# Performance work log

Measured on AMD Instinct MI355X. Metric: run time of the kernel, lower is better.

## Reference

```python
import jax, jax.numpy as jnp
import numpy as np

B, T, E, R, A, M = 64, 2000, 512, 1024, 512, 8


def setup_inputs() -> dict:
    key = jax.random.key(0)
    ks = jax.random.split(key, 9)
    attention_hidden_state = jax.random.normal(ks[0], (B, R), dtype=jnp.float32)
    memory = jax.random.normal(ks[1], (B, T, E), dtype=jnp.float32)
    previous_location = jax.random.uniform(ks[2], (B, 1, M), dtype=jnp.float32) * 10.0
    mask = jnp.zeros((B, T), dtype=bool)
    # F = Linear(R->A, bias, xavier tanh) -> Linear(A->A, no bias, xavier tanh) -> tanh -> lin(A->3M, bias)
    g = 5.0 / 3.0  # tanh gain
    lim1 = g * np.sqrt(6.0 / (R + A))
    W1 = jax.random.uniform(ks[3], (A, R), minval=-lim1, maxval=lim1, dtype=jnp.float32)
    b1 = jnp.zeros((A,), dtype=jnp.float32)
    lim2 = g * np.sqrt(6.0 / (A + A))
    W2 = jax.random.uniform(ks[4], (A, A), minval=-lim2, maxval=lim2, dtype=jnp.float32)
    lim3 = np.sqrt(1.0 / A)
    Wlin = jax.random.uniform(ks[5], (3 * M, A), minval=-lim3, maxval=lim3, dtype=jnp.float32) * 0.01
    blin = jax.random.uniform(ks[6], (3 * M,), minval=-lim3, maxval=lim3, dtype=jnp.float32) * 0.008 - 2.0
    return {"attention_hidden_state": attention_hidden_state, "memory": memory,
            "previous_location": previous_location, "mask": mask,
            "W1": W1, "b1": b1, "W2": W2, "Wlin": Wlin, "blin": blin}


def reference(attention_hidden_state, memory, previous_location, mask, W1, b1, W2, Wlin, blin):
    # normalize_attention_input=True
    h = jnp.tanh(attention_hidden_state)                       # (B, R)
    x = jnp.tanh((h @ W1.T + b1) @ W2.T)                       # (B, A) 2-layer variant
    y = (x @ Wlin.T + blin)[:, None, :]                        # (B, 1, 3M)
    m = y.shape[-1] // 3
    w, delta, scale = y[..., :m], y[..., m:2 * m], y[..., 2 * m:]
    delta = jax.nn.sigmoid(delta)                              # (B, 1, M)
    loc = previous_location + delta                            # (B, 1, M)
    scale = jax.nn.sigmoid(scale) * 2.0 + 1.0                  # (B, 1, M)
    pos = jnp.arange(memory.shape[1], dtype=memory.dtype)[None, :, None]  # (1, T, 1)
    d = loc - pos                                              # (B, T, M)
    z = 0.5 * (jax.lax.erf((d + 0.5) * scale) - jax.lax.erf((d - 0.5) * scale))
    wmix = jax.nn.sigmoid(w)[:, 0, :]                          # (B, M)
    alignment = jnp.einsum('btm,bm->bt', z, wmix)              # (B, T)
    alignment = jnp.where(mask, jnp.zeros((), alignment.dtype), alignment)  # score_mask_value=0
    attention_weights = jax.nn.softmax(alignment, axis=1)      # (B, T)
    attention_context = jnp.einsum('bt,bte->be', attention_weights, memory)  # (B, E)
    return attention_context, attention_weights, loc
```

## Files before the change

### kernel.cpp

```cpp
#include <hip/hip_runtime.h>
#include <math.h>

#define B 64
#define T 2000
#define E 512
#define R 1024
#define A 512
#define M 8

#define NCH 16
#define TCH (T / NCH)
#define NP  (NCH * 4)

typedef float nfloat4 __attribute__((ext_vector_type(4)));

__device__ float g_params[B * 24];
__device__ float g_partials[B * NP * E];
__device__ float g_psum[B * NCH];

__device__ __forceinline__ float sigmoidf_(float x) { return 1.0f / (1.0f + expf(-x)); }
__device__ __forceinline__ float dot4_(float4 a, float4 b) {
    return (a.x * b.x + a.y * b.y) + (a.z * b.z + a.w * b.w);
}

__global__ __launch_bounds__(512) void mlp_kernel(
    const float* __restrict__ ahs, const float* __restrict__ prev_loc,
    const float* __restrict__ W1, const float* __restrict__ b1,
    const float* __restrict__ W2, const float* __restrict__ Wlin,
    const float* __restrict__ blin,
    float* __restrict__ out_loc)
{
    __shared__ float sh_h[R];
    __shared__ float sh_t[A];
    __shared__ float sh_x[A];
    __shared__ float sh_y[3 * M];

    const int b = blockIdx.x;
    const int tid = threadIdx.x;
    const int wave = tid >> 6;
    const int lane = tid & 63;

    for (int k = tid; k < R; k += 512) sh_h[k] = tanhf(ahs[b * R + k]);
    __syncthreads();

    {
        const float4* h4 = (const float4*)sh_h;
        const float4 h0 = h4[lane], h1 = h4[lane + 64],
                     h2 = h4[lane + 128], h3 = h4[lane + 192];
        for (int j = 0; j < 64; j += 2) {
            const int ja = wave * 64 + j;
            const int jb = ja + 1;
            const float4* ra = (const float4*)(W1 + (size_t)ja * R);
            const float4* rb = (const float4*)(W1 + (size_t)jb * R);
            float4 a0 = ra[lane], a1 = ra[lane + 64], a2 = ra[lane + 128], a3 = ra[lane + 192];
            float4 c0 = rb[lane], c1 = rb[lane + 64], c2 = rb[lane + 128], c3 = rb[lane + 192];
            float accA = (dot4_(h0, a0) + dot4_(h1, a1)) + (dot4_(h2, a2) + dot4_(h3, a3));
            float accB = (dot4_(h0, c0) + dot4_(h1, c1)) + (dot4_(h2, c2) + dot4_(h3, c3));
#pragma unroll
            for (int off = 32; off > 0; off >>= 1) {
                accA += __shfl_down(accA, off);
                accB += __shfl_down(accB, off);
            }
            if (lane == 0) {
                sh_t[ja] = accA + b1[ja];
                sh_t[jb] = accB + b1[jb];
            }
        }
    }
    __syncthreads();

    {
        const float4* t4 = (const float4*)sh_t;
        const float4 t0 = t4[lane], t1 = t4[lane + 64];
        for (int j = 0; j < 64; j += 2) {
            const int ja = wave * 64 + j;
            const int jb = ja + 1;
            const float4* ra = (const float4*)(W2 + (size_t)ja * A);
            const float4* rb = (const float4*)(W2 + (size_t)jb * A);
            float4 a0 = ra[lane], a1 = ra[lane + 64];
            float4 c0 = rb[lane], c1 = rb[lane + 64];
            float accA = dot4_(t0, a0) + dot4_(t1, a1);
            float accB = dot4_(t0, c0) + dot4_(t1, c1);
#pragma unroll
            for (int off = 32; off > 0; off >>= 1) {
                accA += __shfl_down(accA, off);
                accB += __shfl_down(accB, off);
            }
            if (lane == 0) {
                sh_x[ja] = tanhf(accA);
                sh_x[jb] = tanhf(accB);
            }
        }
    }
    __syncthreads();

    if (tid < 16 * 3 * M) {
        const int i = tid >> 4;
        const int l16 = tid & 15;
        float s = 0.f;
        for (int k = l16; k < A; k += 16) s += sh_x[k] * Wlin[i * A + k];
        s += __shfl_down(s, 8, 16);
        s += __shfl_down(s, 4, 16);
        s += __shfl_down(s, 2, 16);
        s += __shfl_down(s, 1, 16);
        if (l16 == 0) sh_y[i] = s + blin[i];
    }
    __syncthreads();

    if (tid < M) {
        const int m = tid;
        const float delta = sigmoidf_(sh_y[M + m]);
        const float loc = prev_loc[b * M + m] + delta;
        const float wmix = sigmoidf_(sh_y[m]);
        const float scale = sigmoidf_(sh_y[2 * M + m]) * 2.0f + 1.0f;
        out_loc[b * M + m] = loc;
        g_params[b * 24 + m]      = wmix;
        g_params[b * 24 + 8 + m]  = loc;
        g_params[b * 24 + 16 + m] = scale;
    }
}

__global__ __launch_bounds__(512) void context_align_kernel(
    const float* __restrict__ memory,
    const unsigned char* __restrict__ mask,
    float* __restrict__ out_w)
{
    __shared__ float sh_w[TCH];
    __shared__ float sh_p[24];

    const int b = blockIdx.x;
    const int chunk = blockIdx.y;
    const int tid = threadIdx.x;
    const int t0 = chunk * TCH;

    if (tid < 24) sh_p[tid] = g_params[b * 24 + tid];
    __syncthreads();

    if (tid < TCH) {
        const int t = t0 + tid;
        const float tf = (float)t;
        float v = 0.f;
#pragma unroll
        for (int m = 0; m < M; ++m) {
            const float d = sh_p[8 + m] - tf;
            const float s = sh_p[16 + m];
            v += 0.5f * (erff((d + 0.5f) * s) - erff((d - 0.5f) * s)) * sh_p[m];
        }
        if (mask[b * T + t]) v = 0.f;
        const float e = expf(v);
        sh_w[tid] = e;
        out_w[b * T + t] = e;
    }
    __syncthreads();

    if (tid < 64) {
        float s = 0.f;
        for (int k = tid; k < TCH; k += 64) s += sh_w[k];
#pragma unroll
        for (int off = 32; off > 0; off >>= 1) s += __shfl_down(s, off);
        if (tid == 0) g_psum[b * NCH + chunk] = s;
    }

    const int e4 = tid & 127;
    const int tp = tid >> 7;
    const nfloat4* mem4 = (const nfloat4*)(memory + (size_t)(b * T + t0) * E);

    float acc0 = 0.f, acc1 = 0.f, acc2 = 0.f, acc3 = 0.f;
#pragma unroll 4
    for (int t = tp; t < TCH; t += 4) {
        const float wv = sh_w[t];
        const nfloat4 mv = __builtin_nontemporal_load(&mem4[(size_t)t * (E / 4) + e4]);
        acc0 += wv * mv.x;
        acc1 += wv * mv.y;
        acc2 += wv * mv.z;
        acc3 += wv * mv.w;
    }

    nfloat4 accv = {acc0, acc1, acc2, acc3};
    nfloat4* dst = (nfloat4*)(g_partials + (((size_t)b * NCH + chunk) * 4 + tp) * E);
    dst[e4] = accv;
}

__global__ __launch_bounds__(256) void finalize_kernel(
    float* __restrict__ out_ctx,
    float* __restrict__ out_w)
{
    __shared__ float s_inv;
    const int b = blockIdx.x;
    const int tid = threadIdx.x;

    if (tid < 64) {
        float s = (tid < NCH) ? g_psum[b * NCH + tid] : 0.f;
#pragma unroll
        for (int off = 32; off > 0; off >>= 1) s += __shfl_down(s, off);
        if (tid == 0) s_inv = 1.0f / s;
    }
    __syncthreads();
    const float inv = s_inv;

    if (tid < E / 4) {
        const float4* p = (const float4*)g_partials + (size_t)b * NP * (E / 4) + tid;
        float4 acc = {0.f, 0.f, 0.f, 0.f};
#pragma unroll 8
        for (int c = 0; c < NP; ++c) {
            const float4 v = p[(size_t)c * (E / 4)];
            acc.x += v.x; acc.y += v.y; acc.z += v.z; acc.w += v.w;
        }
        float4 r = {acc.x * inv, acc.y * inv, acc.z * inv, acc.w * inv};
        ((float4*)out_ctx)[b * (E / 4) + tid] = r;
    }

    float4* w4 = (float4*)(out_w + (size_t)b * T);
    for (int i = tid; i < T / 4; i += 256) {
        float4 v = w4[i];
        v.x *= inv; v.y *= inv; v.z *= inv; v.w *= inv;
        w4[i] = v;
    }
}

extern "C" void kernel_launch(void* const* d_in, const int* in_sizes, int n_in,
                              void* d_out, int out_size, void* d_ws, size_t ws_size,
                              hipStream_t stream) {
    const float* ahs      = (const float*)d_in[0];
    const float* memory   = (const float*)d_in[1];
    const float* prev_loc = (const float*)d_in[2];
    const unsigned char* mask = (const unsigned char*)d_in[3];
    const float* W1   = (const float*)d_in[4];
    const float* b1   = (const float*)d_in[5];
    const float* W2   = (const float*)d_in[6];
    const float* Wlin = (const float*)d_in[7];
    const float* blin = (const float*)d_in[8];

    float* out = (float*)d_out;
    float* out_ctx = out;
    float* out_w   = out + B * E;
    float* out_loc = out + B * E + B * T;

    (void)d_ws; (void)ws_size;

    mlp_kernel<<<dim3(B), dim3(512), 0, stream>>>(
        ahs, prev_loc, W1, b1, W2, Wlin, blin, out_loc);

    context_align_kernel<<<dim3(B, NCH), dim3(512), 0, stream>>>(
        memory, mask, out_w);

    finalize_kernel<<<dim3(B), dim3(256), 0, stream>>>(out_ctx, out_w);
}
```

Measured before the change: 430.4 us.

## Fuse MLP with memory sum and apply sparse correction over a truncated alignment window

For positions well past every mixture location the erf difference is zero in float, so the alignment there is 0 and the unnormalized weight is exp(0)=1. The context is therefore rewritten as the plain memory sum plus a correction from only the first tcut positions. The plain sum no longer depends on the MLP, so extra blocks in the same launch stream memory alongside the MLP blocks, and one kernel launch is removed. This risks small numerical differences from the truncation bound, and it relies on the MLP blocks and the streaming blocks being scheduled concurrently.

```diff
diff --git a/kernel.cpp b/kernel.cpp
--- a/kernel.cpp
+++ b/kernel.cpp
@@ -14,29 +14,57 @@
 
 typedef float nfloat4 __attribute__((ext_vector_type(4)));
 
-__device__ float g_params[B * 24];
 __device__ float g_partials[B * NP * E];
-__device__ float g_psum[B * NCH];
+__device__ float g_corr[B * E];
+__device__ float g_zinv[B];
+__device__ int   g_tcut[B];
 
 __device__ __forceinline__ float sigmoidf_(float x) { return 1.0f / (1.0f + expf(-x)); }
 __device__ __forceinline__ float dot4_(float4 a, float4 b) {
     return (a.x * b.x + a.y * b.y) + (a.z * b.z + a.w * b.w);
 }
 
-__global__ __launch_bounds__(512) void mlp_kernel(
+__global__ __launch_bounds__(512, 4) void fused_kernel(
     const float* __restrict__ ahs, const float* __restrict__ prev_loc,
+    const unsigned char* __restrict__ mask,
     const float* __restrict__ W1, const float* __restrict__ b1,
     const float* __restrict__ W2, const float* __restrict__ Wlin,
     const float* __restrict__ blin,
+    const float* __restrict__ memory,
+    float* __restrict__ out_w,
     float* __restrict__ out_loc)
 {
+    const int tid = threadIdx.x;
+
+    if (blockIdx.x >= B) {
+        const int sblk = blockIdx.x - B;
+        const int b = sblk / NCH;
+        const int chunk = sblk - b * NCH;
+        const int e4 = tid & 127;
+        const int tp = tid >> 7;
+        const nfloat4* mem4 = (const nfloat4*)(memory + (size_t)(b * T + chunk * TCH) * E);
+
+        float acc0 = 0.f, acc1 = 0.f, acc2 = 0.f, acc3 = 0.f;
+#pragma unroll 4
+        for (int t = tp; t < TCH; t += 4) {
+            const nfloat4 mv = __builtin_nontemporal_load(&mem4[(size_t)t * (E / 4) + e4]);
+            acc0 += mv.x; acc1 += mv.y; acc2 += mv.z; acc3 += mv.w;
+        }
+        nfloat4 accv = {acc0, acc1, acc2, acc3};
+        nfloat4* dst = (nfloat4*)(g_partials + (((size_t)b * NCH + chunk) * 4 + tp) * E);
+        dst[e4] = accv;
+        return;
+    }
+
     __shared__ float sh_h[R];
     __shared__ float sh_t[A];
     __shared__ float sh_x[A];
     __shared__ float sh_y[3 * M];
+    __shared__ float sh_loc[M], sh_scale[M], sh_wmix[M], sh_tc[M];
+    __shared__ float sh_e[2048];
+    __shared__ int sh_tcut;
 
     const int b = blockIdx.x;
-    const int tid = threadIdx.x;
     const int wave = tid >> 6;
     const int lane = tid & 63;
 
@@ -111,110 +139,74 @@
         const int m = tid;
         const float delta = sigmoidf_(sh_y[M + m]);
         const float loc = prev_loc[b * M + m] + delta;
-        const float wmix = sigmoidf_(sh_y[m]);
         const float scale = sigmoidf_(sh_y[2 * M + m]) * 2.0f + 1.0f;
+        sh_wmix[m]  = sigmoidf_(sh_y[m]);
+        sh_loc[m]   = loc;
+        sh_scale[m] = scale;
+        sh_tc[m]    = loc + 0.5f + 8.0f / scale;
         out_loc[b * M + m] = loc;
-        g_params[b * 24 + m]      = wmix;
-        g_params[b * 24 + 8 + m]  = loc;
-        g_params[b * 24 + 16 + m] = scale;
-    }
-}
-
-__global__ __launch_bounds__(512) void context_align_kernel(
-    const float* __restrict__ memory,
-    const unsigned char* __restrict__ mask,
-    float* __restrict__ out_w)
-{
-    __shared__ float sh_w[TCH];
-    __shared__ float sh_p[24];
-
-    const int b = blockIdx.x;
-    const int chunk = blockIdx.y;
-    const int tid = threadIdx.x;
-    const int t0 = chunk * TCH;
-
-    if (tid < 24) sh_p[tid] = g_params[b * 24 + tid];
-    __syncthreads();
-
-    if (tid < TCH) {
-        const int t = t0 + tid;
+    }
+    __syncthreads();
+
+    if (tid == 0) {
+        float mx = sh_tc[0];
+        for (int m = 1; m < M; ++m) mx = fmaxf(mx, sh_tc[m]);
+        int tc = (int)ceilf(mx);
+        if (tc < 0) tc = 0;
+        if (tc > T) tc = T;
+        sh_tcut = tc;
+        g_tcut[b] = tc;
+    }
+    __syncthreads();
+    const int tcut = sh_tcut;
+
+    for (int t = tid; t < tcut; t += 512) {
         const float tf = (float)t;
         float v = 0.f;
 #pragma unroll
         for (int m = 0; m < M; ++m) {
-            const float d = sh_p[8 + m] - tf;
-            const float s = sh_p[16 + m];
-            v += 0.5f * (erff((d + 0.5f) * s) - erff((d - 0.5f) * s)) * sh_p[m];
+            const float d = sh_loc[m] - tf;
+            const float s = sh_scale[m];
+            v += 0.5f * (erff((d + 0.5f) * s) - erff((d - 0.5f) * s)) * sh_wmix[m];
         }
         if (mask[b * T + t]) v = 0.f;
         const float e = expf(v);
-        sh_w[tid] = e;
+        sh_e[t] = e;
         out_w[b * T + t] = e;
     }
     __syncthreads();
 
-    if (tid < 64) {
+    if (tid == 0) {
         float s = 0.f;
-        for (int k = tid; k < TCH; k += 64) s += sh_w[k];
-#pragma unroll
-        for (int off = 32; off > 0; off >>= 1) s += __shfl_down(s, off);
-        if (tid == 0) g_psum[b * NCH + chunk] = s;
-    }
-
-    const int e4 = tid & 127;
-    const int tp = tid >> 7;
-    const nfloat4* mem4 = (const nfloat4*)(memory + (size_t)(b * T + t0) * E);
-
-    float acc0 = 0.f, acc1 = 0.f, acc2 = 0.f, acc3 = 0.f;
-#pragma unroll 4
-    for (int t = tp; t < TCH; t += 4) {
-        const float wv = sh_w[t];
-        const nfloat4 mv = __builtin_nontemporal_load(&mem4[(size_t)t * (E / 4) + e4]);
-        acc0 += wv * mv.x;
-        acc1 += wv * mv.y;
-        acc2 += wv * mv.z;
-        acc3 += wv * mv.w;
-    }
-
-    nfloat4 accv = {acc0, acc1, acc2, acc3};
-    nfloat4* dst = (nfloat4*)(g_partials + (((size_t)b * NCH + chunk) * 4 + tp) * E);
-    dst[e4] = accv;
-}
-
-__global__ __launch_bounds__(256) void finalize_kernel(
+        for (int t = 0; t < tcut; ++t) s += sh_e[t];
+        g_zinv[b] = 1.0f / (s + (float)(T - tcut));
+    }
+
+    {
+        float c = 0.f;
+        const float* mrow = memory + (size_t)b * T * E + tid;
+        for (int t = 0; t < tcut; ++t) c += (sh_e[t] - 1.0f) * mrow[(size_t)t * E];
+        g_corr[b * E + tid] = c;
+    }
+}
+
+__global__ __launch_bounds__(512) void finalize_kernel(
     float* __restrict__ out_ctx,
     float* __restrict__ out_w)
 {
-    __shared__ float s_inv;
     const int b = blockIdx.x;
     const int tid = threadIdx.x;
-
-    if (tid < 64) {
-        float s = (tid < NCH) ? g_psum[b * NCH + tid] : 0.f;
-#pragma unroll
-        for (int off = 32; off > 0; off >>= 1) s += __shfl_down(s, off);
-        if (tid == 0) s_inv = 1.0f / s;
-    }
-    __syncthreads();
-    const float inv = s_inv;
-
-    if (tid < E / 4) {
-        const float4* p = (const float4*)g_partials + (size_t)b * NP * (E / 4) + tid;
-        float4 acc = {0.f, 0.f, 0.f, 0.f};
+    const float inv = g_zinv[b];
+    const int tcut = g_tcut[b];
+
+    float acc = g_corr[b * E + tid];
+    const float* p = g_partials + (size_t)b * NP * E + tid;
 #pragma unroll 8
-        for (int c = 0; c < NP; ++c) {
-            const float4 v = p[(size_t)c * (E / 4)];
-            acc.x += v.x; acc.y += v.y; acc.z += v.z; acc.w += v.w;
-        }
-        float4 r = {acc.x * inv, acc.y * inv, acc.z * inv, acc.w * inv};
-        ((float4*)out_ctx)[b * (E / 4) + tid] = r;
-    }
-
-    float4* w4 = (float4*)(out_w + (size_t)b * T);
-    for (int i = tid; i < T / 4; i += 256) {
-        float4 v = w4[i];
-        v.x *= inv; v.y *= inv; v.z *= inv; v.w *= inv;
-        w4[i] = v;
+    for (int c = 0; c < NP; ++c) acc += p[(size_t)c * E];
+    out_ctx[b * E + tid] = acc * inv;
+
+    for (int t = tid; t < T; t += 512) {
+        out_w[b * T + t] = (t < tcut) ? out_w[b * T + t] * inv : inv;
     }
 }
 
@@ -238,11 +230,8 @@
 
     (void)d_ws; (void)ws_size;
 
-    mlp_kernel<<<dim3(B), dim3(512), 0, stream>>>(
-        ahs, prev_loc, W1, b1, W2, Wlin, blin, out_loc);
-
-    context_align_kernel<<<dim3(B, NCH), dim3(512), 0, stream>>>(
-        memory, mask, out_w);
-
-    finalize_kernel<<<dim3(B), dim3(256), 0, stream>>>(out_ctx, out_w);
-}
+    fused_kernel<<<dim3(B + B * NCH), dim3(512), 0, stream>>>(
+        ahs, prev_loc, mask, W1, b1, W2, Wlin, blin, memory, out_w, out_loc);
+
+    finalize_kernel<<<dim3(B), dim3(512), 0, stream>>>(out_ctx, out_w);
+}
```

Measured after the change: 409.5 us. -4.9%, faster.
